# Performance work log

Measured on AMD Instinct MI355X. Metric: run time of the kernel, lower is better.

Reference implementation:

```python
import jax, jax.numpy as jnp
import numpy as np

ROI = 5            # roi_size hardcoded in RPFeatureExtractor(..., roi_size=5)
NUM_CLASSES = 80
MEM_SIZE = 1024


def _roi_align(rp, b, boxes):
    # rp: [B,C,H,W]; b: [N] int batch index; boxes: [N,4] xyxy in feature-map coords.
    # torchvision roi_align semantics, spatial_scale=1, aligned=False.
    # Here roi extents are <=1 (normalized boxes), so roi_w/h clamp to 1.0 and the
    # adaptive sampling_ratio = ceil(1/ROI) = 1 sample per bin (bin-center bilinear).
    B, C, H, W = rp.shape
    rpT = jnp.transpose(rp, (0, 2, 3, 1))  # [B,H,W,C]
    x1, y1, x2, y2 = boxes[:, 0], boxes[:, 1], boxes[:, 2], boxes[:, 3]
    roi_w = jnp.maximum(x2 - x1, 1.0)
    roi_h = jnp.maximum(y2 - y1, 1.0)
    g = jnp.arange(ROI, dtype=rp.dtype) + 0.5
    sx = x1[:, None] + g[None, :] * (roi_w / ROI)[:, None]   # [N,ROI]
    sy = y1[:, None] + g[None, :] * (roi_h / ROI)[:, None]   # [N,ROI]
    N = boxes.shape[0]
    x = jnp.broadcast_to(sx[:, None, :], (N, ROI, ROI))
    y = jnp.broadcast_to(sy[:, :, None], (N, ROI, ROI))
    invalid = (y < -1.0) | (y > H) | (x < -1.0) | (x > W)
    y = jnp.maximum(y, 0.0)
    x = jnp.maximum(x, 0.0)
    yl = jnp.floor(y).astype(jnp.int32)
    xl = jnp.floor(x).astype(jnp.int32)
    y = jnp.where(yl >= H - 1, jnp.asarray(H - 1, rp.dtype), y)
    x = jnp.where(xl >= W - 1, jnp.asarray(W - 1, rp.dtype), x)
    yl = jnp.minimum(yl, H - 1)
    xl = jnp.minimum(xl, W - 1)
    yh = jnp.minimum(yl + 1, H - 1)
    xh = jnp.minimum(xl + 1, W - 1)
    ly = (y - yl.astype(rp.dtype))[..., None]
    lx = (x - xl.astype(rp.dtype))[..., None]
    hy, hx = 1.0 - ly, 1.0 - lx
    bb = b[:, None, None]
    v = (rpT[bb, yl, xl] * hy * hx + rpT[bb, yl, xh] * hy * lx
         + rpT[bb, yh, xl] * ly * hx + rpT[bb, yh, xh] * ly * lx)  # [N,ROI,ROI,C]
    v = jnp.where(invalid[..., None], jnp.asarray(0.0, rp.dtype), v)
    # torch output is [N,C,ROI,ROI] flattened -> transpose before reshape
    return jnp.transpose(v, (0, 3, 1, 2)).reshape(N, -1)


def _project_and_normalize(feats, w1, b1, w2, b2):
    h = jax.nn.relu(feats @ w1.T + b1)
    f = h @ w2.T + b2
    f = f + 1e-8                                   # source adds eps before normalize
    n = jnp.linalg.norm(f, axis=1, keepdims=True)
    return f / jnp.maximum(n, 1e-12)               # F.normalize semantics


def _update_memory(feat_norm, cls, memory_bank, memory_count, class_freq):
    feats_d = jax.lax.stop_gradient(feat_norm)     # .detach() in source
    onehot = (cls[:, None] == jnp.arange(NUM_CLASSES)[None, :]).astype(jnp.int32)
    occ = jnp.cumsum(onehot, axis=0) - onehot      # exclusive per-class rank
    occ_i = jnp.take_along_axis(occ, cls[:, None].astype(jnp.int32), axis=1)[:, 0]
    pos = (memory_count[cls] + occ_i) % MEM_SIZE
    flat = cls.astype(jnp.int32) * MEM_SIZE + pos
    dim = memory_bank.shape[-1]
    mb = memory_bank.reshape(NUM_CLASSES * MEM_SIZE, dim).at[flat].set(feats_d)
    mb = mb.reshape(NUM_CLASSES, MEM_SIZE, dim)
    per_cls = jnp.sum(onehot, axis=0)
    count_new = memory_count + per_cls
    freq_new = class_freq + per_cls.astype(class_freq.dtype)
    total = jnp.sum(freq_new)
    prob = jnp.clip(freq_new / total, 1e-8, None)
    cw = 1.0 / jnp.sqrt(prob + 1e-8)
    cw = cw / cw.mean()
    return mb, count_new, freq_new, cw


def setup_inputs() -> dict:
    key = jax.random.key(0)
    ks = jax.random.split(key, 8)
    B, C, H, W, N = 16, 256, 128, 128, 512
    enc, hid, dim = C * ROI * ROI, 2048, 256
    return {
        "rp_features": jax.random.normal(ks[0], (B, C, H, W), jnp.float32),
        "batch_idx": jax.random.randint(ks[1], (N,), 0, B, jnp.int32),
        "cls": jax.random.randint(ks[2], (N,), 0, NUM_CLASSES, jnp.int32),
        "bboxes": jax.random.uniform(ks[3], (N, 4), jnp.float32),  # normalized xywh
        "img_h": 640,
        "img_w": 640,
        "w1": jax.random.normal(ks[4], (hid, enc), jnp.float32) * 0.02,
        "b1": jnp.zeros((hid,), jnp.float32),
        "w2": jax.random.normal(ks[5], (dim, hid), jnp.float32) * 0.02,
        "b2": jnp.zeros((dim,), jnp.float32),
        "memory_bank": jnp.zeros((NUM_CLASSES, MEM_SIZE, dim), jnp.float32),
        "memory_count": jnp.zeros((NUM_CLASSES,), jnp.int32),
        "class_freq": jnp.zeros((NUM_CLASSES,), jnp.float32),
    }


def reference(rp_features, batch_idx, cls, bboxes, img_h, img_w,
              w1, b1, w2, b2, memory_bank, memory_count, class_freq):
    # xywh (normalized) -> xyxy; source scales by img_size then divides it back
    # inside extract_roi_features, so boxes end up in [0,1] feature-map coords.
    cx, cy, w, h = bboxes[:, 0], bboxes[:, 1], bboxes[:, 2], bboxes[:, 3]
    boxes = jnp.stack([cx - w / 2, cy - h / 2, cx + w / 2, cy + h / 2], axis=1)
    # valid_mask (x2>x1 & y2>y1) always true here since w,h > 0 by construction.
    feats = _roi_align(rp_features, batch_idx, boxes)           # [N, C*25]
    feat_norm = _project_and_normalize(feats, w1, b1, w2, b2)   # [N, 256]
    mb, count_new, freq_new, cw = _update_memory(
        feat_norm, cls, memory_bank, memory_count, class_freq)
    return feat_norm, mb, count_new, cw
```

## Files before the change

kernel.cpp:

```cpp
#include <hip/hip_runtime.h>

#define NBOX 512
#define ENC 6400
#define HID 2048
#define DIM 256
#define NCLS 80
#define MEMSZ 1024
#define Bm 16
#define Cc 256
#define Hh 128
#define Ww 128

typedef __attribute__((ext_vector_type(8))) short bf16x8;
typedef __attribute__((ext_vector_type(4))) float f32x4;

__device__ __forceinline__ ushort f2bf(float x) {
  union { float f; unsigned u; } v;
  v.f = x;
  const unsigned r = v.u + 0x7fffu + ((v.u >> 16) & 1u);
  return (ushort)(r >> 16);
}

__global__ __launch_bounds__(256) void roi_scan_kernel(
    const float* __restrict__ rp, const int* __restrict__ bidx,
    const float* __restrict__ bboxes, ushort* __restrict__ feats, int N,
    const int* __restrict__ cls, const int* __restrict__ mcount,
    const float* __restrict__ cfreq, int* __restrict__ pos,
    float* __restrict__ outCNT, float* __restrict__ outCW) {
  const int n = blockIdx.x;
  if (n == N) {
    __shared__ int scls[NBOX];
    __shared__ float sf[NCLS], sc[NCLS];
    __shared__ float s_tot, s_mean;
    const int t = threadIdx.x;
    if (t < 128) *(int4*)&scls[t * 4] = *(const int4*)&cls[t * 4];
    __syncthreads();
    if (t < NCLS) {
      int cnt = 0;
      const int base = mcount[t];
      for (int i = 0; i < N; ++i) {
        if (scls[i] == t) { pos[i] = (base + cnt) % MEMSZ; ++cnt; }
      }
      outCNT[t] = (float)(base + cnt);
      sf[t] = cfreq[t] + (float)cnt;
    }
    __syncthreads();
    if (t == 0) {
      float s = 0.0f;
      for (int i = 0; i < NCLS; ++i) s += sf[i];
      s_tot = s;
    }
    __syncthreads();
    if (t < NCLS) sc[t] = 1.0f / sqrtf(fmaxf(sf[t] / s_tot, 1e-8f) + 1e-8f);
    __syncthreads();
    if (t == 0) {
      float s = 0.0f;
      for (int i = 0; i < NCLS; ++i) s += sc[i];
      s_mean = s / (float)NCLS;
    }
    __syncthreads();
    if (t < NCLS) outCW[t] = sc[t] / s_mean;
    return;
  }
  const int b = bidx[n];
  const float cx = bboxes[n * 4 + 0], cy = bboxes[n * 4 + 1];
  const float bw = bboxes[n * 4 + 2], bh = bboxes[n * 4 + 3];
  const float x1 = cx - bw * 0.5f, y1 = cy - bh * 0.5f;
  const float x2 = cx + bw * 0.5f, y2 = cy + bh * 0.5f;
  const float roi_w = fmaxf(x2 - x1, 1.0f), roi_h = fmaxf(y2 - y1, 1.0f);
  const float stx = roi_w / 5.0f, sty = roi_h / 5.0f;
  for (int j4 = threadIdx.x; j4 < ENC / 4; j4 += 256) {
    ushort4 o;
    float ov[4];
#pragma unroll
    for (int e = 0; e < 4; ++e) {
      const int j = j4 * 4 + e;
      const int c = j / 25, p = j % 25, gy = p / 5, gx = p % 5;
      const float sx = x1 + ((float)gx + 0.5f) * stx;
      const float sy = y1 + ((float)gy + 0.5f) * sty;
      const bool invalid = (sy < -1.0f) || (sy > (float)Hh) || (sx < -1.0f) || (sx > (float)Ww);
      float v = 0.0f;
      if (!invalid) {
        float y = fmaxf(sy, 0.0f), x = fmaxf(sx, 0.0f);
        int yl = (int)floorf(y), xl = (int)floorf(x);
        if (yl >= Hh - 1) y = (float)(Hh - 1);
        if (xl >= Ww - 1) x = (float)(Ww - 1);
        yl = min(yl, Hh - 1);
        xl = min(xl, Ww - 1);
        const int yh = min(yl + 1, Hh - 1), xh = min(xl + 1, Ww - 1);
        const float ly = y - (float)yl, lx = x - (float)xl;
        const float hy = 1.0f - ly, hx = 1.0f - lx;
        const float* base = rp + ((long)(b * Cc + c) << 14);
        const float v00 = base[(yl << 7) + xl];
        const float v01 = base[(yl << 7) + xh];
        const float v10 = base[(yh << 7) + xl];
        const float v11 = base[(yh << 7) + xh];
        v = v00 * hy * hx + v01 * hy * lx + v10 * ly * hx + v11 * ly * lx;
      }
      ov[e] = v;
    }
    o.x = f2bf(ov[0]); o.y = f2bf(ov[1]); o.z = f2bf(ov[2]); o.w = f2bf(ov[3]);
    *(ushort4*)(feats + (long)n * ENC + j4 * 4) = o;
  }
}

__global__ __launch_bounds__(256) void gemm1_splitk(
    const ushort* __restrict__ A, const float* __restrict__ B,
    float* __restrict__ P,
    const float4* __restrict__ csrc, float4* __restrict__ cdst, int cn4) {
  const int tid = threadIdx.x;
  constexpr int ZG = 5;
  if ((int)blockIdx.z >= ZG) {
    const int nb = 64 * ((int)gridDim.z - ZG);
    const int cb = (((int)blockIdx.z - ZG) * 4 + (int)blockIdx.y) * 16 + (int)blockIdx.x;
    const int base = (cb * 256 + tid) * 4;
    const int stride = nb * 256 * 4;
    for (int i = base; i + 3 < cn4; i += stride) {
      const float4 a0 = csrc[i], a1 = csrc[i + 1], a2 = csrc[i + 2], a3 = csrc[i + 3];
      cdst[i] = a0; cdst[i + 1] = a1; cdst[i + 2] = a2; cdst[i + 3] = a3;
    }
    return;
  }
  __shared__ ushort lds[2][16384];
  const int lane = tid & 63;
  const int wave = tid >> 6;
  const int wr = wave >> 1, wc = wave & 1;
  const int m0 = blockIdx.y * 128, n0 = blockIdx.x * 128;
  const long kz = (long)blockIdx.z * 1280;

  f32x4 acc[4][4];
#pragma unroll
  for (int i = 0; i < 4; ++i)
#pragma unroll
    for (int j = 0; j < 4; ++j) acc[i][j] = (f32x4)0.0f;

  int4 aR[4];
  float4 bR[8];

  auto G_load = [&](int kt) {
#pragma unroll
    for (int p = 0; p < 4; ++p) {
      const int cid = tid + p * 256;
      const int row = cid >> 3, c = cid & 7;
      aR[p] = *(const int4*)(A + (long)(m0 + row) * ENC + kz + kt + c * 8);
      const float* bp = B + (long)(n0 + row) * ENC + kz + kt + c * 8;
      bR[p * 2] = *(const float4*)bp;
      bR[p * 2 + 1] = *(const float4*)(bp + 4);
    }
  };
  auto L_store = [&](int buf) {
    ushort* Ab = &lds[buf][0];
    ushort* Bb = &lds[buf][8192];
#pragma unroll
    for (int p = 0; p < 4; ++p) {
      const int cid = tid + p * 256;
      const int row = cid >> 3, c = (cid & 7) ^ (row & 7);
      *(int4*)&Ab[row * 64 + c * 8] = aR[p];
      ushort4 lo, hi;
      lo.x = f2bf(bR[p * 2].x); lo.y = f2bf(bR[p * 2].y);
      lo.z = f2bf(bR[p * 2].z); lo.w = f2bf(bR[p * 2].w);
      hi.x = f2bf(bR[p * 2 + 1].x); hi.y = f2bf(bR[p * 2 + 1].y);
      hi.z = f2bf(bR[p * 2 + 1].z); hi.w = f2bf(bR[p * 2 + 1].w);
      *(ushort4*)&Bb[row * 64 + c * 8] = lo;
      *(ushort4*)&Bb[row * 64 + c * 8 + 4] = hi;
    }
  };

  const int lr = lane & 15;
  const int g = lane >> 4;
  constexpr int NT = 20;

  G_load(0);
  L_store(0);
  __syncthreads();
  for (int t = 0; t < NT; ++t) {
    const int cur = t & 1;
    if (t + 1 < NT) G_load((t + 1) * 64);
    const ushort* Ab = &lds[cur][0];
    const ushort* Bb = &lds[cur][8192];
#pragma unroll
    for (int h0 = 0; h0 < 2; ++h0) {
      bf16x8 a[4], b[4];
#pragma unroll
      for (int i = 0; i < 4; ++i) {
        const int row = wr * 64 + i * 16 + lr;
        a[i] = *(const bf16x8*)&Ab[row * 64 + ((h0 * 4 + g) ^ (row & 7)) * 8];
      }
#pragma unroll
      for (int j = 0; j < 4; ++j) {
        const int row = wc * 64 + j * 16 + lr;
        b[j] = *(const bf16x8*)&Bb[row * 64 + ((h0 * 4 + g) ^ (row & 7)) * 8];
      }
#pragma unroll
      for (int i = 0; i < 4; ++i)
#pragma unroll
        for (int j = 0; j < 4; ++j)
          acc[i][j] = __builtin_amdgcn_mfma_f32_16x16x32_bf16(a[i], b[j], acc[i][j], 0, 0, 0);
    }
    if (t + 1 < NT) L_store(cur ^ 1);
    __syncthreads();
  }

  float* Pp = P + (long)blockIdx.z * NBOX * HID;
  const int r0 = m0 + wr * 64 + ((lane >> 4) << 2);
  const int c0 = n0 + wc * 64 + lr;
#pragma unroll
  for (int i = 0; i < 4; ++i)
#pragma unroll
    for (int j = 0; j < 4; ++j)
#pragma unroll
      for (int r = 0; r < 4; ++r)
        Pp[(long)(r0 + i * 16 + r) * HID + c0 + j * 16] = acc[i][j][r];
}

__global__ __launch_bounds__(256) void reduce_bias_relu_bf16(
    const float* __restrict__ P, const float* __restrict__ bias,
    ushort* __restrict__ out, int MN, int Ncols, int Z) {
  const int e = (blockIdx.x * 256 + threadIdx.x) * 4;
  if (e >= MN) return;
  float4 s = *(const float4*)(P + e);
  for (int z = 1; z < Z; ++z) {
    const float4 t = *(const float4*)(P + (long)z * MN + e);
    s.x += t.x; s.y += t.y; s.z += t.z; s.w += t.w;
  }
  const float4 bb = *(const float4*)(bias + (e & (Ncols - 1)));
  ushort4 o;
  o.x = f2bf(fmaxf(s.x + bb.x, 0.0f));
  o.y = f2bf(fmaxf(s.y + bb.y, 0.0f));
  o.z = f2bf(fmaxf(s.z + bb.z, 0.0f));
  o.w = f2bf(fmaxf(s.w + bb.w, 0.0f));
  *(ushort4*)(out + e) = o;
}

template <int BM, int BN, int WM, int WN, int TM, int TN>
__global__ __launch_bounds__(WM * WN * 64) void gemm_bf16_nt(
    const ushort* __restrict__ A, const float* __restrict__ B,
    float* __restrict__ P, int M, int N, int K, int kchunk) {
  constexpr int THREADS = WM * WN * 64;
  const int tid = threadIdx.x;
  constexpr int CA = BM * 4 / THREADS;
  constexpr int CB = BN * 8 / THREADS;
  __shared__ ushort As[2][BM][40];
  __shared__ ushort Bs[2][BN][40];
  const int lane = tid & 63;
  const int wave = tid >> 6;
  const int wr = wave / WN, wc = wave % WN;
  const int m0 = blockIdx.y * BM, n0 = blockIdx.x * BN;
  const long kz = (long)blockIdx.z * kchunk;

  f32x4 acc[TM][TN];
#pragma unroll
  for (int i = 0; i < TM; ++i)
#pragma unroll
    for (int j = 0; j < TN; ++j) acc[i][j] = (f32x4)0.0f;

  int4 areg[CA];
  float4 breg[CB];

  auto loadt = [&](int kt) {
#pragma unroll
    for (int i = 0; i < CA; ++i) {
      const int f = tid + i * THREADS;
      areg[i] = *(const int4*)(A + (long)(m0 + (f >> 2)) * K + kz + kt + (f & 3) * 8);
    }
#pragma unroll
    for (int i = 0; i < CB; ++i) {
      const int f = tid + i * THREADS;
      breg[i] = *(const float4*)(B + (long)(n0 + (f >> 3)) * K + kz + kt + (f & 7) * 4);
    }
  };
  auto storet = [&](int buf) {
#pragma unroll
    for (int i = 0; i < CA; ++i) {
      const int f = tid + i * THREADS;
      *(int4*)&As[buf][f >> 2][(f & 3) * 8] = areg[i];
    }
#pragma unroll
    for (int i = 0; i < CB; ++i) {
      const int f = tid + i * THREADS;
      const float4 bv = breg[i];
      ushort4 o;
      o.x = f2bf(bv.x); o.y = f2bf(bv.y); o.z = f2bf(bv.z); o.w = f2bf(bv.w);
      *(ushort4*)&Bs[buf][f >> 3][(f & 7) * 4] = o;
    }
  };

  const int lrow = lane & 15;
  const int kb = (lane >> 4) * 8;
  const int NT = kchunk / 32;

  loadt(0);
  storet(0);
  __syncthreads();
  for (int t = 0; t < NT; ++t) {
    const int cur = t & 1;
    if (t + 1 < NT) loadt((t + 1) * 32);
    bf16x8 a[TM], b[TN];
#pragma unroll
    for (int i = 0; i < TM; ++i)
      a[i] = *(const bf16x8*)&As[cur][wr * (TM * 16) + i * 16 + lrow][kb];
#pragma unroll
    for (int j = 0; j < TN; ++j)
      b[j] = *(const bf16x8*)&Bs[cur][wc * (TN * 16) + j * 16 + lrow][kb];
#pragma unroll
    for (int i = 0; i < TM; ++i)
#pragma unroll
      for (int j = 0; j < TN; ++j)
        acc[i][j] = __builtin_amdgcn_mfma_f32_16x16x32_bf16(a[i], b[j], acc[i][j], 0, 0, 0);
    if (t + 1 < NT) storet(cur ^ 1);
    __syncthreads();
  }

  float* Pp = P + (long)blockIdx.z * M * N;
  const int r0 = m0 + wr * (TM * 16) + ((lane >> 4) << 2);
  const int c0 = n0 + wc * (TN * 16) + lrow;
#pragma unroll
  for (int i = 0; i < TM; ++i)
#pragma unroll
    for (int j = 0; j < TN; ++j)
#pragma unroll
      for (int r = 0; r < 4; ++r)
        Pp[(long)(r0 + i * 16 + r) * N + c0 + j * 16] = acc[i][j][r];
}

__global__ __launch_bounds__(256) void reduce_norm_scatter(
    const float* __restrict__ P, const float* __restrict__ b2,
    float* __restrict__ outFN, float* __restrict__ outMB,
    const int* __restrict__ cls, const int* __restrict__ pos, int M, int Z) {
  const int m = blockIdx.x, d = threadIdx.x;
  float f = 0.0f;
  for (int z = 0; z < Z; ++z) f += P[((long)z * M + m) * DIM + d];
  f += b2[d] + 1e-8f;
  float ss = f * f;
#pragma unroll
  for (int o = 32; o > 0; o >>= 1) ss += __shfl_xor(ss, o, 64);
  __shared__ float sred[4];
  if ((d & 63) == 0) sred[d >> 6] = ss;
  __syncthreads();
  const float tot = sred[0] + sred[1] + sred[2] + sred[3];
  const float nrm = fmaxf(sqrtf(tot), 1e-12f);
  const float r = f / nrm;
  outFN[(long)m * DIM + d] = r;
  outMB[((long)cls[m] * MEMSZ + pos[m]) * DIM + d] = r;
}

extern "C" void kernel_launch(void* const* d_in, const int* in_sizes, int n_in,
                              void* d_out, int out_size, void* d_ws, size_t ws_size,
                              hipStream_t stream) {
  const float* rp = (const float*)d_in[0];
  const int* bidx = (const int*)d_in[1];
  const int* cls = (const int*)d_in[2];
  const float* bboxes = (const float*)d_in[3];
  const float* w1 = (const float*)d_in[6];
  const float* b1 = (const float*)d_in[7];
  const float* w2 = (const float*)d_in[8];
  const float* b2 = (const float*)d_in[9];
  const float* mbank = (const float*)d_in[10];
  const int* mcount = (const int*)d_in[11];
  const float* cfreq = (const float*)d_in[12];
  const int N = in_sizes[1];

  char* ws = (char*)d_ws;
  ushort* feats = (ushort*)ws;
  float* P1 = (float*)(ws + 6553600);
  ushort* h = (ushort*)(ws + 6553600 + 20971520);
  int* pos = (int*)(ws + 6553600 + 20971520 + 2097152);
  float* P2 = P1;

  float* outFN = (float*)d_out;
  float* outMB = outFN + (long)NBOX * DIM;
  float* outCNT = outMB + (long)NCLS * MEMSZ * DIM;
  float* outCW = outCNT + NCLS;

  roi_scan_kernel<<<N + 1, 256, 0, stream>>>(rp, bidx, bboxes, feats, N,
                                             cls, mcount, cfreq, pos, outCNT, outCW);

  gemm1_splitk<<<dim3(HID / 128, NBOX / 128, 13), 256, 0, stream>>>(
      feats, w1, P1, (const float4*)mbank, (float4*)outMB, NCLS * MEMSZ * DIM / 4);

  reduce_bias_relu_bf16<<<NBOX * HID / 4 / 256, 256, 0, stream>>>(
      P1, b1, h, NBOX * HID, HID, 5);

  gemm_bf16_nt<128, 64, 2, 2, 4, 2><<<dim3(DIM / 64, NBOX / 128, 8), 256, 0, stream>>>(
      h, w2, P2, NBOX, DIM, HID, HID / 8);

  reduce_norm_scatter<<<NBOX, 256, 0, stream>>>(P2, b2, outFN, outMB, cls, pos, NBOX, 8);
}
```

Measured before the change: 131.2 us.

## Pre-convert w1 to bf16 in ROI kernel and double-prefetch GEMM1 loads

```diff
diff --git a/kernel.cpp b/kernel.cpp
--- a/kernel.cpp
+++ b/kernel.cpp
@@ -21,13 +21,28 @@
   return (ushort)(r >> 16);
 }
 
-__global__ __launch_bounds__(256) void roi_scan_kernel(
+__global__ __launch_bounds__(256) void roi_scan_conv_kernel(
     const float* __restrict__ rp, const int* __restrict__ bidx,
     const float* __restrict__ bboxes, ushort* __restrict__ feats, int N,
     const int* __restrict__ cls, const int* __restrict__ mcount,
     const float* __restrict__ cfreq, int* __restrict__ pos,
-    float* __restrict__ outCNT, float* __restrict__ outCW) {
+    float* __restrict__ outCNT, float* __restrict__ outCW,
+    const float* __restrict__ w1f, ushort* __restrict__ w1b) {
   const int n = blockIdx.x;
+  if (n > N) {
+    const int wt = (n - N - 1) * 256 + (int)threadIdx.x;
+    const int nchunk = HID * ENC / 8;
+    for (int i = wt; i < nchunk; i += 384 * 256) {
+      const float4 f0 = *(const float4*)(w1f + (long)i * 8);
+      const float4 f1 = *(const float4*)(w1f + (long)i * 8 + 4);
+      ushort4 lo, hi;
+      lo.x = f2bf(f0.x); lo.y = f2bf(f0.y); lo.z = f2bf(f0.z); lo.w = f2bf(f0.w);
+      hi.x = f2bf(f1.x); hi.y = f2bf(f1.y); hi.z = f2bf(f1.z); hi.w = f2bf(f1.w);
+      *(ushort4*)(w1b + (long)i * 8) = lo;
+      *(ushort4*)(w1b + (long)i * 8 + 4) = hi;
+    }
+    return;
+  }
   if (n == N) {
     __shared__ int scls[NBOX];
     __shared__ float sf[NCLS], sc[NCLS];
@@ -105,7 +120,7 @@
 }
 
 __global__ __launch_bounds__(256) void gemm1_splitk(
-    const ushort* __restrict__ A, const float* __restrict__ B,
+    const ushort* __restrict__ A, const ushort* __restrict__ Bb16,
     float* __restrict__ P,
     const float4* __restrict__ csrc, float4* __restrict__ cdst, int cn4) {
   const int tid = threadIdx.x;
@@ -134,35 +149,29 @@
 #pragma unroll
     for (int j = 0; j < 4; ++j) acc[i][j] = (f32x4)0.0f;
 
-  int4 aR[4];
-  float4 bR[8];
-
-  auto G_load = [&](int kt) {
+  int4 aR0[4], bR0[4], aR1[4], bR1[4];
+
+  auto G_load = [&](int set, int kt) {
 #pragma unroll
     for (int p = 0; p < 4; ++p) {
       const int cid = tid + p * 256;
       const int row = cid >> 3, c = cid & 7;
-      aR[p] = *(const int4*)(A + (long)(m0 + row) * ENC + kz + kt + c * 8);
-      const float* bp = B + (long)(n0 + row) * ENC + kz + kt + c * 8;
-      bR[p * 2] = *(const float4*)bp;
-      bR[p * 2 + 1] = *(const float4*)(bp + 4);
+      const long off = (long)row * ENC + kz + kt + c * 8;
+      const int4 av = *(const int4*)(A + (long)m0 * ENC + off);
+      const int4 bv = *(const int4*)(Bb16 + (long)n0 * ENC + off);
+      if (set == 0) { aR0[p] = av; bR0[p] = bv; }
+      else          { aR1[p] = av; bR1[p] = bv; }
     }
   };
-  auto L_store = [&](int buf) {
+  auto L_store = [&](int buf, int set) {
     ushort* Ab = &lds[buf][0];
     ushort* Bb = &lds[buf][8192];
 #pragma unroll
     for (int p = 0; p < 4; ++p) {
       const int cid = tid + p * 256;
       const int row = cid >> 3, c = (cid & 7) ^ (row & 7);
-      *(int4*)&Ab[row * 64 + c * 8] = aR[p];
-      ushort4 lo, hi;
-      lo.x = f2bf(bR[p * 2].x); lo.y = f2bf(bR[p * 2].y);
-      lo.z = f2bf(bR[p * 2].z); lo.w = f2bf(bR[p * 2].w);
-      hi.x = f2bf(bR[p * 2 + 1].x); hi.y = f2bf(bR[p * 2 + 1].y);
-      hi.z = f2bf(bR[p * 2 + 1].z); hi.w = f2bf(bR[p * 2 + 1].w);
-      *(ushort4*)&Bb[row * 64 + c * 8] = lo;
-      *(ushort4*)&Bb[row * 64 + c * 8 + 4] = hi;
+      *(int4*)&Ab[row * 64 + c * 8] = (set == 0) ? aR0[p] : aR1[p];
+      *(int4*)&Bb[row * 64 + c * 8] = (set == 0) ? bR0[p] : bR1[p];
     }
   };
 
@@ -170,12 +179,15 @@
   const int g = lane >> 4;
   constexpr int NT = 20;
 
-  G_load(0);
-  L_store(0);
-  __syncthreads();
+  G_load(0, 0);
+  L_store(0, 0);
+  G_load(1, 64);
+  asm volatile("s_waitcnt lgkmcnt(0)" ::: "memory");
+  __builtin_amdgcn_s_barrier();
+
   for (int t = 0; t < NT; ++t) {
     const int cur = t & 1;
-    if (t + 1 < NT) G_load((t + 1) * 64);
+    if (t + 2 < NT) G_load(cur, (t + 2) * 64);
     const ushort* Ab = &lds[cur][0];
     const ushort* Bb = &lds[cur][8192];
 #pragma unroll
@@ -197,8 +209,9 @@
         for (int j = 0; j < 4; ++j)
           acc[i][j] = __builtin_amdgcn_mfma_f32_16x16x32_bf16(a[i], b[j], acc[i][j], 0, 0, 0);
     }
-    if (t + 1 < NT) L_store(cur ^ 1);
-    __syncthreads();
+    if (t + 1 < NT) L_store(cur ^ 1, (t + 1) & 1);
+    asm volatile("s_waitcnt lgkmcnt(0)" ::: "memory");
+    __builtin_amdgcn_s_barrier();
   }
 
   float* Pp = P + (long)blockIdx.z * NBOX * HID;
@@ -365,6 +378,7 @@
   float* P1 = (float*)(ws + 6553600);
   ushort* h = (ushort*)(ws + 6553600 + 20971520);
   int* pos = (int*)(ws + 6553600 + 20971520 + 2097152);
+  ushort* w1b = (ushort*)(ws + 6553600 + 20971520 + 2097152 + 2048);
   float* P2 = P1;
 
   float* outFN = (float*)d_out;
@@ -372,11 +386,11 @@
   float* outCNT = outMB + (long)NCLS * MEMSZ * DIM;
   float* outCW = outCNT + NCLS;
 
-  roi_scan_kernel<<<N + 1, 256, 0, stream>>>(rp, bidx, bboxes, feats, N,
-                                             cls, mcount, cfreq, pos, outCNT, outCW);
+  roi_scan_conv_kernel<<<N + 1 + 384, 256, 0, stream>>>(
+      rp, bidx, bboxes, feats, N, cls, mcount, cfreq, pos, outCNT, outCW, w1, w1b);
 
   gemm1_splitk<<<dim3(HID / 128, NBOX / 128, 13), 256, 0, stream>>>(
-      feats, w1, P1, (const float4*)mbank, (float4*)outMB, NCLS * MEMSZ * DIM / 4);
+      feats, w1b, P1, (const float4*)mbank, (float4*)outMB, NCLS * MEMSZ * DIM / 4);
 
   reduce_bias_relu_bf16<<<NBOX * HID / 4 / 256, 256, 0, stream>>>(
       P1, b1, h, NBOX * HID, HID, 5);
```

New measurement: 210.0 us. 1.6x slower.
